# Optimization experiments

Measured on AMD Instinct MI355X. Metric: run time of the kernel, lower is better.

The kernel has to match this reference:

```python
import jax, jax.numpy as jnp
import numpy as np

N, T, D, H = 256, 256, 1024, 1024


def setup_inputs() -> dict:
    key = jax.random.key(0)
    k1, k2, k3, k4, k5, k6 = jax.random.split(key, 6)
    encoded_subjects = jax.random.normal(k1, (N, T, D), dtype=jnp.float32)
    encoded_objects = jax.random.normal(k2, (N, T, D), dtype=jnp.float32)
    # pair_ffn: Linear(2D -> H), ReLU, Linear(H -> 1); torch Linear stores W as [out, in]
    lim1 = 1.0 / np.sqrt(2 * D)
    W1 = jax.random.uniform(k3, (H, 2 * D), dtype=jnp.float32, minval=-lim1, maxval=lim1)
    b1 = jax.random.uniform(k4, (H,), dtype=jnp.float32, minval=-lim1, maxval=lim1)
    lim2 = 1.0 / np.sqrt(H)
    W2 = jax.random.uniform(k5, (1, H), dtype=jnp.float32, minval=-lim2, maxval=lim2)
    b2 = jax.random.uniform(k6, (1,), dtype=jnp.float32, minval=-lim2, maxval=lim2)
    return {
        "encoded_subjects": encoded_subjects,
        "encoded_objects": encoded_objects,
        "W1": W1,
        "b1": b1,
        "W2": W2,
        "b2": b2,
    }


def reference(encoded_subjects, encoded_objects, W1, b1, W2, b2):
    # max-pool over token dim -> [N, D]
    sub = jnp.max(encoded_subjects, axis=1)
    obj = jnp.max(encoded_objects, axis=1)
    n = obj.shape[0]
    # cat([sub_i, obj_j]) @ W1.T == sub_i @ W1[:, :D].T + obj_j @ W1[:, D:].T
    d = sub.shape[-1]
    s_part = jnp.einsum("nd,hd->nh", sub, W1[:, :d])  # [N, H]
    o_part = jnp.einsum("nd,hd->nh", obj, W1[:, d:])  # [N, H]
    h = jax.nn.relu(s_part[:, None, :] + o_part[None, :, :] + b1)  # [N, N, H]
    scores = jnp.einsum("ijh,h->ij", h, W2[0]) + b2[0]  # [N, N]
    # diagonal entries stay zero (loop skips i == j)
    pair_matrix = jnp.where(jnp.eye(n, dtype=bool), 0.0, scores)
    return pair_matrix
```

## Files before the change

### kernel.cpp

```cpp
#include <hip/hip_runtime.h>
#include <math.h>

#define NN 256
#define TT 256
#define DD 1024
#define HH 1024

typedef float f32x4 __attribute__((ext_vector_type(4)));
typedef short bf16x8 __attribute__((ext_vector_type(8)));

__device__ inline unsigned short f2bf_rne(float x) {
    unsigned u = __float_as_uint(x);
    unsigned r = (u + 0x7fffu + ((u >> 16) & 1u)) >> 16;
    return (unsigned short)r;
}
__device__ inline float bf2f(unsigned short h) {
    return __uint_as_float(((unsigned)h) << 16);
}

__global__ __launch_bounds__(256) void pool_kernel(const float* __restrict__ subs,
                                                   const float* __restrict__ objs,
                                                   float* __restrict__ pooled) {
    const int n = blockIdx.x;
    const int which = blockIdx.y;
    const f32x4* src = reinterpret_cast<const f32x4*>(which == 0 ? subs : objs);
    const int d4 = threadIdx.x;
    const f32x4* base = src + (((size_t)n) << 16) + d4;

    f32x4 a[8];
#pragma unroll
    for (int s = 0; s < 8; ++s) a[s] = (f32x4){-INFINITY, -INFINITY, -INFINITY, -INFINITY};

    for (int k = 0; k < 256; k += 8) {
        f32x4 v[8];
#pragma unroll
        for (int s = 0; s < 8; ++s)
            v[s] = __builtin_nontemporal_load(base + (size_t)(k + s) * 256);
#pragma unroll
        for (int s = 0; s < 8; ++s) {
#pragma unroll
            for (int e = 0; e < 4; ++e) a[s][e] = fmaxf(a[s][e], v[s][e]);
        }
    }
#pragma unroll
    for (int s = 0; s < 4; ++s)
#pragma unroll
        for (int e = 0; e < 4; ++e) a[s][e] = fmaxf(a[s][e], a[s + 4][e]);
    f32x4 m;
#pragma unroll
    for (int e = 0; e < 4; ++e)
        m[e] = fmaxf(fmaxf(a[0][e], a[1][e]), fmaxf(a[2][e], a[3][e]));

    reinterpret_cast<f32x4*>(pooled)[((size_t)(which * NN + n)) * 256 + d4] = m;
}

__global__ __launch_bounds__(256, 1) void gemm_kernel(const float* __restrict__ A,
                                                      const float* __restrict__ W1,
                                                      const float* __restrict__ b1,
                                                      float* __restrict__ out) {
    __shared__ unsigned short Ah[64 * 40];
    __shared__ unsigned short Al[64 * 40];
    __shared__ unsigned short Bh[32 * 40];
    __shared__ unsigned short Bl[32 * 40];

    const int t = threadIdx.x;
    const int lane = t & 63;
    const int w = t >> 6;
    const int wm = w >> 1, wn = w & 1;
    const int n0 = blockIdx.x * 32;
    const int m0 = blockIdx.y * 64;
    const bool is_sub = (m0 < NN);
    const int koff = is_sub ? 0 : DD;

    const int ar = t >> 2;
    const int akq = (t & 3) * 8;
    const int br = (t & 127) >> 2;
    const int bkq = akq;

    f32x4 acc0 = {0.f, 0.f, 0.f, 0.f};
    f32x4 acc1 = {0.f, 0.f, 0.f, 0.f};

    const int iA0 = (wm * 32 + (lane & 15)) * 40 + (lane >> 4) * 8;
    const int iA1 = (wm * 32 + 16 + (lane & 15)) * 40 + (lane >> 4) * 8;
    const int iB  = (wn * 16 + (lane & 15)) * 40 + (lane >> 4) * 8;

    for (int ch = 0; ch < 32; ++ch) {
        const int kb = ch * 32;
        const float* ap = A + (size_t)(m0 + ar) * DD + kb + akq;
        f32x4 av0 = *(const f32x4*)ap;
        f32x4 av1 = *(const f32x4*)(ap + 4);
        f32x4 bv0, bv1;
        if (t < 128) {
            const float* bp = W1 + (size_t)(n0 + br) * (2 * DD) + koff + kb + bkq;
            bv0 = *(const f32x4*)bp;
            bv1 = *(const f32x4*)(bp + 4);
        }
        __syncthreads();

        {
            float xs[8];
#pragma unroll
            for (int e = 0; e < 4; ++e) { xs[e] = av0[e]; xs[4 + e] = av1[e]; }
            unsigned hw[4], lw[4];
#pragma unroll
            for (int p = 0; p < 4; ++p) {
                unsigned short h0 = f2bf_rne(xs[2 * p]);
                unsigned short h1 = f2bf_rne(xs[2 * p + 1]);
                unsigned short l0 = f2bf_rne(xs[2 * p] - bf2f(h0));
                unsigned short l1 = f2bf_rne(xs[2 * p + 1] - bf2f(h1));
                hw[p] = (unsigned)h0 | ((unsigned)h1 << 16);
                lw[p] = (unsigned)l0 | ((unsigned)l1 << 16);
            }
            *(uint4*)&Ah[ar * 40 + akq] = make_uint4(hw[0], hw[1], hw[2], hw[3]);
            *(uint4*)&Al[ar * 40 + akq] = make_uint4(lw[0], lw[1], lw[2], lw[3]);
        }
        if (t < 128) {
            float xs[8];
#pragma unroll
            for (int e = 0; e < 4; ++e) { xs[e] = bv0[e]; xs[4 + e] = bv1[e]; }
            unsigned hw[4], lw[4];
#pragma unroll
            for (int p = 0; p < 4; ++p) {
                unsigned short h0 = f2bf_rne(xs[2 * p]);
                unsigned short h1 = f2bf_rne(xs[2 * p + 1]);
                unsigned short l0 = f2bf_rne(xs[2 * p] - bf2f(h0));
                unsigned short l1 = f2bf_rne(xs[2 * p + 1] - bf2f(h1));
                hw[p] = (unsigned)h0 | ((unsigned)h1 << 16);
                lw[p] = (unsigned)l0 | ((unsigned)l1 << 16);
            }
            *(uint4*)&Bh[br * 40 + bkq] = make_uint4(hw[0], hw[1], hw[2], hw[3]);
            *(uint4*)&Bl[br * 40 + bkq] = make_uint4(lw[0], lw[1], lw[2], lw[3]);
        }
        __syncthreads();

        bf16x8 a0h = *(const bf16x8*)&Ah[iA0];
        bf16x8 a0l = *(const bf16x8*)&Al[iA0];
        bf16x8 a1h = *(const bf16x8*)&Ah[iA1];
        bf16x8 a1l = *(const bf16x8*)&Al[iA1];
        bf16x8 bh  = *(const bf16x8*)&Bh[iB];
        bf16x8 bl  = *(const bf16x8*)&Bl[iB];

        acc0 = __builtin_amdgcn_mfma_f32_16x16x32_bf16(a0h, bh, acc0, 0, 0, 0);
        acc0 = __builtin_amdgcn_mfma_f32_16x16x32_bf16(a0h, bl, acc0, 0, 0, 0);
        acc0 = __builtin_amdgcn_mfma_f32_16x16x32_bf16(a0l, bh, acc0, 0, 0, 0);
        acc1 = __builtin_amdgcn_mfma_f32_16x16x32_bf16(a1h, bh, acc1, 0, 0, 0);
        acc1 = __builtin_amdgcn_mfma_f32_16x16x32_bf16(a1h, bl, acc1, 0, 0, 0);
        acc1 = __builtin_amdgcn_mfma_f32_16x16x32_bf16(a1l, bh, acc1, 0, 0, 0);
    }

    const int col = n0 + wn * 16 + (lane & 15);
    const float bias = is_sub ? b1[col] : 0.f;
    const int rb = m0 + wm * 32 + (lane >> 4) * 4;
#pragma unroll
    for (int r = 0; r < 4; ++r) {
        out[(size_t)(rb + r) * HH + col] = acc0[r] + bias;
        out[(size_t)(rb + 16 + r) * HH + col] = acc1[r] + bias;
    }
}

#define HC 128

__global__ __launch_bounds__(256) void pair_kernel(const float* __restrict__ sp_op,
                                                   const float* __restrict__ W2,
                                                   const float* __restrict__ b2,
                                                   float* __restrict__ out) {
    __shared__ float sT[16][HC + 4];
    __shared__ float oT[16][HC + 4];
    const int t = threadIdx.x;
    const int tx = t & 15, ty = t >> 4;
    const int i0 = blockIdx.y * 16, j0 = blockIdx.x * 16;
    const float* sp = sp_op;
    const float* op = sp_op + (size_t)NN * HH;

    const int s_row = t >> 5;
    const int s_h = (t & 31) * 4;

    float4 rs[2], ro[2];
#pragma unroll
    for (int r = 0; r < 2; ++r) {
        const int row = s_row + r * 8;
        rs[r] = *(const float4*)&sp[(size_t)(i0 + row) * HH + s_h];
        ro[r] = *(const float4*)&op[(size_t)(j0 + row) * HH + s_h];
    }

    float acc = 0.f;
    for (int c = 0; c < HH / HC; ++c) {
#pragma unroll
        for (int r = 0; r < 2; ++r) {
            const int row = s_row + r * 8;
            *(float4*)&sT[row][s_h] = rs[r];
            *(float4*)&oT[row][s_h] = ro[r];
        }
        float4 ns[2], no[2];
        if (c + 1 < HH / HC) {
#pragma unroll
            for (int r = 0; r < 2; ++r) {
                const int row = s_row + r * 8;
                ns[r] = *(const float4*)&sp[(size_t)(i0 + row) * HH + (c + 1) * HC + s_h];
                no[r] = *(const float4*)&op[(size_t)(j0 + row) * HH + (c + 1) * HC + s_h];
            }
        }
        __syncthreads();
#pragma unroll
        for (int h4 = 0; h4 < HC / 4; ++h4) {
            float4 s = *(const float4*)&sT[ty][h4 * 4];
            float4 o = *(const float4*)&oT[tx][h4 * 4];
            float4 w = *(const float4*)&W2[c * HC + h4 * 4];
            acc += fmaxf(s.x + o.x, 0.f) * w.x;
            acc += fmaxf(s.y + o.y, 0.f) * w.y;
            acc += fmaxf(s.z + o.z, 0.f) * w.z;
            acc += fmaxf(s.w + o.w, 0.f) * w.w;
        }
        __syncthreads();
        if (c + 1 < HH / HC) {
#pragma unroll
            for (int r = 0; r < 2; ++r) { rs[r] = ns[r]; ro[r] = no[r]; }
        }
    }
    const int i = i0 + ty, j = j0 + tx;
    const float score = acc + b2[0];
    out[i * NN + j] = (i == j) ? 0.f : score;
}

extern "C" void kernel_launch(void* const* d_in, const int* in_sizes, int n_in,
                              void* d_out, int out_size, void* d_ws, size_t ws_size,
                              hipStream_t stream) {
    const float* subs = (const float*)d_in[0];
    const float* objs = (const float*)d_in[1];
    const float* W1   = (const float*)d_in[2];
    const float* b1   = (const float*)d_in[3];
    const float* W2   = (const float*)d_in[4];
    const float* b2   = (const float*)d_in[5];
    float* out = (float*)d_out;

    float* pooled = (float*)d_ws;
    float* sp_op  = pooled + (size_t)2 * NN * DD;

    pool_kernel<<<dim3(NN, 2), 256, 0, stream>>>(subs, objs, pooled);
    gemm_kernel<<<dim3(HH / 32, (2 * NN) / 64), 256, 0, stream>>>(pooled, W1, b1, sp_op);
    pair_kernel<<<dim3(NN / 16, NN / 16), 256, 0, stream>>>(sp_op, W2, b2, out);
}
```

Baseline: 145.3 us.

## Prefetch GEMM tiles, deepen pool loads, and register-block pair kernel

The pool kernel now issues 16 nontemporal loads per iteration instead of 8, to raise memory-level parallelism on the dominant streaming reduction. The GEMM kernel software-prefetches the next K-chunk of A and W1 into registers before the barrier, overlapping global loads with the conversion and MFMA work. The pair kernel halves its thread count and computes two output columns per thread, reusing each shared-memory s row and W2 load, and writes a float2. The costs are more register pressure and fewer threads per pair block.

Result: slower. 156.7 us (+7.9%).

```diff
diff --git a/kernel.cpp b/kernel.cpp
--- a/kernel.cpp
+++ b/kernel.cpp
@@ -31,15 +31,15 @@
 #pragma unroll
     for (int s = 0; s < 8; ++s) a[s] = (f32x4){-INFINITY, -INFINITY, -INFINITY, -INFINITY};
 
-    for (int k = 0; k < 256; k += 8) {
-        f32x4 v[8];
-#pragma unroll
-        for (int s = 0; s < 8; ++s)
+    for (int k = 0; k < 256; k += 16) {
+        f32x4 v[16];
+#pragma unroll
+        for (int s = 0; s < 16; ++s)
             v[s] = __builtin_nontemporal_load(base + (size_t)(k + s) * 256);
 #pragma unroll
-        for (int s = 0; s < 8; ++s) {
-#pragma unroll
-            for (int e = 0; e < 4; ++e) a[s][e] = fmaxf(a[s][e], v[s][e]);
+        for (int s = 0; s < 16; ++s) {
+#pragma unroll
+            for (int e = 0; e < 4; ++e) a[s & 7][e] = fmaxf(a[s & 7][e], v[s][e]);
         }
     }
 #pragma unroll
@@ -77,6 +77,9 @@
     const int br = (t & 127) >> 2;
     const int bkq = akq;
 
+    const float* apb = A + (size_t)(m0 + ar) * DD + akq;
+    const float* bpb = W1 + (size_t)(n0 + br) * (2 * DD) + koff + bkq;
+
     f32x4 acc0 = {0.f, 0.f, 0.f, 0.f};
     f32x4 acc1 = {0.f, 0.f, 0.f, 0.f};
 
@@ -84,16 +87,24 @@
     const int iA1 = (wm * 32 + 16 + (lane & 15)) * 40 + (lane >> 4) * 8;
     const int iB  = (wn * 16 + (lane & 15)) * 40 + (lane >> 4) * 8;
 
+    f32x4 av0 = *(const f32x4*)apb;
+    f32x4 av1 = *(const f32x4*)(apb + 4);
+    f32x4 bv0 = {0,0,0,0}, bv1 = {0,0,0,0};
+    if (t < 128) {
+        bv0 = *(const f32x4*)bpb;
+        bv1 = *(const f32x4*)(bpb + 4);
+    }
+
     for (int ch = 0; ch < 32; ++ch) {
-        const int kb = ch * 32;
-        const float* ap = A + (size_t)(m0 + ar) * DD + kb + akq;
-        f32x4 av0 = *(const f32x4*)ap;
-        f32x4 av1 = *(const f32x4*)(ap + 4);
-        f32x4 bv0, bv1;
-        if (t < 128) {
-            const float* bp = W1 + (size_t)(n0 + br) * (2 * DD) + koff + kb + bkq;
-            bv0 = *(const f32x4*)bp;
-            bv1 = *(const f32x4*)(bp + 4);
+        f32x4 nav0, nav1, nbv0, nbv1;
+        if (ch < 31) {
+            const int kg = (ch + 1) * 32;
+            nav0 = *(const f32x4*)(apb + kg);
+            nav1 = *(const f32x4*)(apb + kg + 4);
+            if (t < 128) {
+                nbv0 = *(const f32x4*)(bpb + kg);
+                nbv1 = *(const f32x4*)(bpb + kg + 4);
+            }
         }
         __syncthreads();
 
@@ -146,6 +157,8 @@
         acc1 = __builtin_amdgcn_mfma_f32_16x16x32_bf16(a1h, bh, acc1, 0, 0, 0);
         acc1 = __builtin_amdgcn_mfma_f32_16x16x32_bf16(a1h, bl, acc1, 0, 0, 0);
         acc1 = __builtin_amdgcn_mfma_f32_16x16x32_bf16(a1l, bh, acc1, 0, 0, 0);
+
+        av0 = nav0; av1 = nav1; bv0 = nbv0; bv1 = nbv1;
     }
 
     const int col = n0 + wn * 16 + (lane & 15);
@@ -160,14 +173,15 @@
 
 #define HC 128
 
-__global__ __launch_bounds__(256) void pair_kernel(const float* __restrict__ sp_op,
+__global__ __launch_bounds__(128) void pair_kernel(const float* __restrict__ sp_op,
                                                    const float* __restrict__ W2,
                                                    const float* __restrict__ b2,
                                                    float* __restrict__ out) {
     __shared__ float sT[16][HC + 4];
     __shared__ float oT[16][HC + 4];
     const int t = threadIdx.x;
-    const int tx = t & 15, ty = t >> 4;
+    const int txp = t & 7;
+    const int ty = t >> 3;
     const int i0 = blockIdx.y * 16, j0 = blockIdx.x * 16;
     const float* sp = sp_op;
     const float* op = sp_op + (size_t)NN * HH;
@@ -175,27 +189,27 @@
     const int s_row = t >> 5;
     const int s_h = (t & 31) * 4;
 
-    float4 rs[2], ro[2];
-#pragma unroll
-    for (int r = 0; r < 2; ++r) {
-        const int row = s_row + r * 8;
+    float4 rs[4], ro[4];
+#pragma unroll
+    for (int r = 0; r < 4; ++r) {
+        const int row = s_row + r * 4;
         rs[r] = *(const float4*)&sp[(size_t)(i0 + row) * HH + s_h];
         ro[r] = *(const float4*)&op[(size_t)(j0 + row) * HH + s_h];
     }
 
-    float acc = 0.f;
+    float acc0 = 0.f, acc1 = 0.f;
     for (int c = 0; c < HH / HC; ++c) {
 #pragma unroll
-        for (int r = 0; r < 2; ++r) {
-            const int row = s_row + r * 8;
+        for (int r = 0; r < 4; ++r) {
+            const int row = s_row + r * 4;
             *(float4*)&sT[row][s_h] = rs[r];
             *(float4*)&oT[row][s_h] = ro[r];
         }
-        float4 ns[2], no[2];
+        float4 ns[4], no[4];
         if (c + 1 < HH / HC) {
 #pragma unroll
-            for (int r = 0; r < 2; ++r) {
-                const int row = s_row + r * 8;
+            for (int r = 0; r < 4; ++r) {
+                const int row = s_row + r * 4;
                 ns[r] = *(const float4*)&sp[(size_t)(i0 + row) * HH + (c + 1) * HC + s_h];
                 no[r] = *(const float4*)&op[(size_t)(j0 + row) * HH + (c + 1) * HC + s_h];
             }
@@ -203,23 +217,31 @@
         __syncthreads();
 #pragma unroll
         for (int h4 = 0; h4 < HC / 4; ++h4) {
-            float4 s = *(const float4*)&sT[ty][h4 * 4];
-            float4 o = *(const float4*)&oT[tx][h4 * 4];
-            float4 w = *(const float4*)&W2[c * HC + h4 * 4];
-            acc += fmaxf(s.x + o.x, 0.f) * w.x;
-            acc += fmaxf(s.y + o.y, 0.f) * w.y;
-            acc += fmaxf(s.z + o.z, 0.f) * w.z;
-            acc += fmaxf(s.w + o.w, 0.f) * w.w;
+            float4 s  = *(const float4*)&sT[ty][h4 * 4];
+            float4 o0 = *(const float4*)&oT[txp * 2][h4 * 4];
+            float4 o1 = *(const float4*)&oT[txp * 2 + 1][h4 * 4];
+            float4 w  = *(const float4*)&W2[c * HC + h4 * 4];
+            acc0 += fmaxf(s.x + o0.x, 0.f) * w.x;
+            acc0 += fmaxf(s.y + o0.y, 0.f) * w.y;
+            acc0 += fmaxf(s.z + o0.z, 0.f) * w.z;
+            acc0 += fmaxf(s.w + o0.w, 0.f) * w.w;
+            acc1 += fmaxf(s.x + o1.x, 0.f) * w.x;
+            acc1 += fmaxf(s.y + o1.y, 0.f) * w.y;
+            acc1 += fmaxf(s.z + o1.z, 0.f) * w.z;
+            acc1 += fmaxf(s.w + o1.w, 0.f) * w.w;
         }
         __syncthreads();
         if (c + 1 < HH / HC) {
 #pragma unroll
-            for (int r = 0; r < 2; ++r) { rs[r] = ns[r]; ro[r] = no[r]; }
-        }
-    }
-    const int i = i0 + ty, j = j0 + tx;
-    const float score = acc + b2[0];
-    out[i * NN + j] = (i == j) ? 0.f : score;
+            for (int r = 0; r < 4; ++r) { rs[r] = ns[r]; ro[r] = no[r]; }
+        }
+    }
+    const int i = i0 + ty, j = j0 + txp * 2;
+    const float b = b2[0];
+    float2 res;
+    res.x = (i == j) ? 0.f : acc0 + b;
+    res.y = (i == j + 1) ? 0.f : acc1 + b;
+    *(float2*)&out[i * NN + j] = res;
 }
 
 extern "C" void kernel_launch(void* const* d_in, const int* in_sizes, int n_in,
@@ -238,5 +260,5 @@
 
     pool_kernel<<<dim3(NN, 2), 256, 0, stream>>>(subs, objs, pooled);
     gemm_kernel<<<dim3(HH / 32, (2 * NN) / 64), 256, 0, stream>>>(pooled, W1, b1, sp_op);
-    pair_kernel<<<dim3(NN / 16, NN / 16), 256, 0, stream>>>(sp_op, W2, b2, out);
-}
+    pair_kernel<<<dim3(NN / 16, NN / 16), 128, 0, stream>>>(sp_op, W2, b2, out);
+}
```
